# Optimization experiments

Measured on AMD Instinct MI355X. Metric: run time of the kernel, lower is better.

Reference implementation:

```python
import jax, jax.numpy as jnp
import numpy as np

ALPHA = 0.25
GAMMA = 2.0
EPS = 1e-8


def _lsa(cost):
    """Jonker-Volgenant shortest-augmenting-path linear sum assignment.
    Matches scipy.optimize.linear_sum_assignment for rectangular matrices."""
    cost = np.asarray(cost, dtype=np.float64)
    transposed = cost.shape[0] > cost.shape[1]
    if transposed:
        cost = cost.T
    n, m = cost.shape  # n <= m
    INF = 1e18
    u = np.zeros(n + 1)
    v = np.zeros(m + 1)
    p = np.zeros(m + 1, dtype=np.int64)   # p[j] = row (1-indexed) assigned to col j
    way = np.zeros(m + 1, dtype=np.int64)
    for i in range(1, n + 1):
        p[0] = i
        j0 = 0
        minv = np.full(m + 1, INF)
        used = np.zeros(m + 1, dtype=bool)
        while True:
            used[j0] = True
            i0 = p[j0]
            cur = cost[i0 - 1] - u[i0] - v[1:]
            free = ~used[1:]
            better = free & (cur < minv[1:])
            minv[1:][better] = cur[better]
            way[1:][better] = j0
            masked = np.where(free, minv[1:], INF)
            j1 = int(np.argmin(masked)) + 1
            delta = masked[j1 - 1]
            u[p[used]] += delta
            v[used] -= delta
            minv[1:][free] -= delta
            j0 = j1
            if p[j0] == 0:
                break
        while j0 != 0:  # augment
            j1 = way[j0]
            p[j0] = p[j1]
            j0 = j1
    row_of_col = p[1:] - 1
    cols = np.nonzero(row_of_col >= 0)[0]
    rows = row_of_col[cols]
    if transposed:
        rows, cols = cols, rows
    order = np.argsort(rows)
    return rows[order], cols[order]


def _focal_cost(p):
    """pos_cost - neg_cost for sigmoid probs p, per focal-loss matcher cost."""
    neg = (1.0 - ALPHA) * p ** GAMMA * (-jnp.log(1.0 - p + EPS))
    pos = ALPHA * (1.0 - p) ** GAMMA * (-jnp.log(p + EPS))
    return pos - neg


def _match(rec, loc, targets):
    """rec: [bs, Q, Crec] logits; loc: [bs, Q, Cloc] logits; targets: [bs, nt] int.
    Returns (src_idx, tgt_idx) each [bs, nt] (query index, target index)."""
    nt = targets.shape[1]
    cost_class = jnp.take_along_axis(_focal_cost(jax.nn.sigmoid(rec)),
                                     targets[:, None, :], axis=2)      # [bs, Q, nt]
    cost_pos = _focal_cost(jax.nn.sigmoid(loc))[:, :, :nt]             # tgt_pos = arange(nt)
    C = np.asarray(2.0 * cost_class + cost_pos)                        # [bs, Q, nt]
    src, tgt = [], []
    for b in range(C.shape[0]):  # per-batch Hungarian, as in original
        r, c = _lsa(C[b])
        src.append(r)
        tgt.append(c)
    return jnp.asarray(np.stack(src)), jnp.asarray(np.stack(tgt))


def _ce(logits, labels):
    # F.cross_entropy with mean reduction
    logp = jax.nn.log_softmax(logits, axis=-1)
    return -jnp.mean(jnp.take_along_axis(logp, labels[..., None], axis=-1))


def setup_inputs() -> dict:
    key = jax.random.key(0)
    k1, k2, k3 = jax.random.split(key, 3)
    rec = jax.random.normal(k1, (128, 107, 32, 32), dtype=jnp.float32)
    loc = jax.random.normal(k2, (128, 25, 32, 32), dtype=jnp.float32)
    targets = jax.random.randint(k3, (128, 25), 0, 107, dtype=jnp.int64)
    return {"rec": rec, "loc": loc, "targets": targets}


def reference(rec, loc, targets):
    bs, c_rec, H, W = rec.shape
    c_loc = loc.shape[1]
    nt = targets.shape[1]
    rec = jnp.transpose(rec.reshape(bs, c_rec, H * W), (0, 2, 1))  # [bs, Q, Crec]
    loc = jnp.transpose(loc.reshape(bs, c_loc, H * W), (0, 2, 1))  # [bs, Q, Cloc]
    src_idx, tgt_idx = _match(rec, loc, targets)                   # [bs, nt] each
    rec_m = jnp.take_along_axis(rec, src_idx[:, :, None], axis=1)  # [bs, nt, Crec]
    loc_m = jnp.take_along_axis(loc, src_idx[:, :, None], axis=1)  # [bs, nt, Cloc]
    cls_labels = jnp.take_along_axis(targets, tgt_idx, axis=1)     # [bs, nt]
    pos_labels = tgt_idx                                           # tgt_pos[b, j] == j
    det_rec_losses = _ce(rec_m.reshape(bs * nt, c_rec), cls_labels.reshape(-1))
    pos_losses = _ce(loc_m.reshape(bs * nt, c_loc), pos_labels.reshape(-1))
    return (det_rec_losses, pos_losses)
```

## Files before the change

kernel.cpp:

```cpp
#include <hip/hip_runtime.h>
#include <hip/hip_bf16.h>
#include <math.h>

#define BS   128
#define NT   25
#define CREC 107
#define CLOC 25
#define QN   1024
#define INFD 1e18
#define WSTR 257
__device__ __forceinline__ int widx(int j) {
    int q = j - 1;
    return (q & 3) * WSTR + (q >> 2);
}

__device__ __forceinline__ float focal_cost_f(float x) {
    float p   = 1.0f / (1.0f + __expf(-x));
    float neg = 0.75f * p * p * (-__logf(1.0f - p + 1e-8f));
    float pos = 0.25f * (1.0f - p) * (1.0f - p) * (-__logf(p + 1e-8f));
    return pos - neg;
}

__global__ __launch_bounds__(256)
void rowmin_kernel(const float* __restrict__ rec, const float* __restrict__ loc,
                   const int* __restrict__ targets, float* __restrict__ cost_g,
                   float* __restrict__ rowmin_g, int* __restrict__ rowarg_g) {
    const int pid   = blockIdx.x;
    const int b     = pid / NT, r = pid % NT;
    const int tid   = threadIdx.x;
    const int qbase = tid << 2;
    const int tc    = targets[pid];

    float4 r4 = *(const float4*)(rec + ((size_t)b * CREC + tc) * QN + qbase);
    float4 l4 = *(const float4*)(loc + ((size_t)b * CLOC + r)  * QN + qbase);
    float4 c;
    c.x = 2.0f * focal_cost_f(r4.x) + focal_cost_f(l4.x);
    c.y = 2.0f * focal_cost_f(r4.y) + focal_cost_f(l4.y);
    c.z = 2.0f * focal_cost_f(r4.z) + focal_cost_f(l4.z);
    c.w = 2.0f * focal_cost_f(r4.w) + focal_cost_f(l4.w);
    *(float4*)(cost_g + ((size_t)pid << 10) + qbase) = c;

    float bv = c.x; int bq = qbase;
    if (c.y < bv) { bv = c.y; bq = qbase + 1; }
    if (c.z < bv) { bv = c.z; bq = qbase + 2; }
    if (c.w < bv) { bv = c.w; bq = qbase + 3; }
    #pragma unroll
    for (int off = 32; off; off >>= 1) {
        float ov = __shfl_xor(bv, off);
        int   oq = __shfl_xor(bq, off);
        if (ov < bv || (ov == bv && oq < bq)) { bv = ov; bq = oq; }
    }
    __shared__ float bmv[4];
    __shared__ int   bmq[4];
    if ((tid & 63) == 0) { bmv[tid >> 6] = bv; bmq[tid >> 6] = bq; }
    __syncthreads();
    if (tid == 0) {
        float fv = bmv[0]; int fq = bmq[0];
        #pragma unroll
        for (int w = 1; w < 4; ++w) {
            float ov = bmv[w]; int oq = bmq[w];
            if (ov < fv || (ov == fv && oq < fq)) { fv = ov; fq = oq; }
        }
        rowmin_g[pid] = fv; rowarg_g[pid] = fq;
    }
}

__global__ __launch_bounds__(256)
void search_kernel(const float* __restrict__ cost_g,
                   const float* __restrict__ rowmin_g, const int* __restrict__ rowarg_g,
                   int* __restrict__ pairq_g) {
    const int b     = blockIdx.x;
    const int tid   = threadIdx.x;
    const int wave  = tid >> 6;
    const int lane  = tid & 63;
    const int qbase = tid << 2;

    __shared__ int    way_s[4 * WSTR];
    __shared__ int    p_s[QN + 1];
    __shared__ double u_s[NT + 1];
    __shared__ float  rowmin_s[NT];
    __shared__ int    rowarg_s[NT];
    __shared__ int    unassigned_s[NT];
    __shared__ int    nun_s;
    __shared__ double candv_s[2][4];
    __shared__ int    candj_s[2][4];

    for (int j = tid; j <= QN; j += 256) p_s[j] = 0;
    if (tid < NT) {
        rowmin_s[tid] = rowmin_g[b * NT + tid];
        rowarg_s[tid] = rowarg_g[b * NT + tid];
    }
    __syncthreads();

    if (tid == 0) {
        nun_s = 0;
        for (int r = 0; r < NT; ++r) {
            u_s[r + 1] = (double)rowmin_s[r];
            int j = rowarg_s[r] + 1;
            if (p_s[j] == 0) p_s[j] = r + 1;
            else             unassigned_s[nun_s++] = r + 1;
        }
    }
    __syncthreads();
    const int nun = nun_s;

    const float* cb = cost_g + ((size_t)b * NT << 10);

    double v[4] = {0.0, 0.0, 0.0, 0.0};

    for (int s = 0; s < nun; ++s) {
        const int i = unassigned_s[s];
        double minv[4] = {INFD, INFD, INFD, INFD};
        double snap[4] = {0.0, 0.0, 0.0, 0.0};
        double dsum    = 0.0;
        unsigned usedmask = 0;
        int j0 = 0;
        int parity = 0;

        for (;;) {
            int i0;
            if (j0 == 0) {
                i0 = i;
            } else {
                int q0 = j0 - 1;
                if ((q0 >> 2) == tid) {
                    int m = q0 & 3;
                    usedmask |= 1u << m;
                    minv[m] = INFD;
                    snap[m] = dsum;
                }
                i0 = p_s[j0];
            }
            const double ui0 = u_s[i0];
            const float4 c4 = *(const float4*)(cb + ((size_t)(i0 - 1) << 10) + qbase);
            const float cf[4] = { c4.x, c4.y, c4.z, c4.w };

            double bestv = INFD; int bestj = QN + 2;
            #pragma unroll
            for (int m = 0; m < 4; ++m) {
                if (!(usedmask & (1u << m))) {
                    const int j = qbase + m + 1;
                    double cur = (double)cf[m] - ui0 - v[m];
                    if (cur < minv[m]) { minv[m] = cur; way_s[widx(j)] = j0; }
                    double mv = minv[m];
                    if (mv < bestv || (mv == bestv && j < bestj)) { bestv = mv; bestj = j; }
                }
            }

            float own32 = (float)bestv;
            float w32 = own32;
            #pragma unroll
            for (int off = 32; off; off >>= 1) w32 = fminf(w32, __shfl_xor(w32, off));
            unsigned long long cand = __ballot(own32 == w32);
            double wv = INFD; int wj = QN + 2;
            while (cand) {
                int l = __ffsll(cand) - 1; cand &= cand - 1;
                double vv = __shfl(bestv, l);
                int    jj = __shfl(bestj, l);
                if (vv < wv || (vv == wv && jj < wj)) { wv = vv; wj = jj; }
            }
            if (lane == 0) { candv_s[parity][wave] = wv; candj_s[parity][wave] = wj; }
            __syncthreads();
            double delta = candv_s[parity][0]; int j1 = candj_s[parity][0];
            #pragma unroll
            for (int w = 1; w < 4; ++w) {
                double dv = candv_s[parity][w]; int dj = candj_s[parity][w];
                if (dv < delta || (dv == delta && dj < j1)) { delta = dv; j1 = dj; }
            }
            parity ^= 1;
            dsum += delta;

            #pragma unroll
            for (int m = 0; m < 4; ++m) {
                if (usedmask & (1u << m)) v[m]    -= delta;
                else                      minv[m] -= delta;
            }
            j0 = j1;
            if (p_s[j0] == 0) break;
        }

        if (tid == 0) u_s[i] += dsum;
        unsigned mm = usedmask;
        while (mm) {
            int m = __ffs(mm) - 1; mm &= mm - 1;
            u_s[p_s[qbase + m + 1]] += dsum - snap[m];
        }
        __syncthreads();
        if (tid == 0) {
            int jj = j0;
            while (jj != 0) {
                int jn = way_s[widx(jj)];
                p_s[jj] = (jn == 0) ? i : p_s[jn];
                jj = jn;
            }
        }
        __syncthreads();
    }

    for (int j = tid + 1; j <= QN; j += 256)
        if (p_s[j] > 0) pairq_g[b * NT + (p_s[j] - 1)] = j - 1;
}

__global__ __launch_bounds__(64)
void loss_kernel(const float* __restrict__ rec, const float* __restrict__ loc,
                 const int* __restrict__ targets, const int* __restrict__ pairq_g,
                 float* __restrict__ partial) {
    const int pid  = blockIdx.x;
    const int b    = pid / NT, t = pid % NT;
    const int lane = threadIdx.x;
    const int q    = pairq_g[pid];

    const float* rb = rec + (size_t)b * CREC * QN + q;
    float x0 = (lane < CREC)      ? rb[(size_t)lane * QN]        : -1e30f;
    float x1 = (lane + 64 < CREC) ? rb[(size_t)(lane + 64) * QN] : -1e30f;
    float mx = fmaxf(x0, x1);
    #pragma unroll
    for (int off = 32; off; off >>= 1) mx = fmaxf(mx, __shfl_xor(mx, off));
    float e = 0.0f;
    if (lane < CREC)      e += expf(x0 - mx);
    if (lane + 64 < CREC) e += expf(x1 - mx);
    #pragma unroll
    for (int off = 32; off; off >>= 1) e += __shfl_xor(e, off);
    float lse = mx + logf(e);

    const float* lb = loc + (size_t)b * CLOC * QN + q;
    float y = (lane < CLOC) ? lb[(size_t)lane * QN] : -1e30f;
    float my = y;
    #pragma unroll
    for (int off = 32; off; off >>= 1) my = fmaxf(my, __shfl_xor(my, off));
    float ey = (lane < CLOC) ? expf(y - my) : 0.0f;
    #pragma unroll
    for (int off = 32; off; off >>= 1) ey += __shfl_xor(ey, off);
    float lsey = my + logf(ey);

    if (lane == 0) {
        int lab = targets[pid];
        partial[pid]           = lse  - rb[(size_t)lab * QN];
        partial[BS * NT + pid] = lsey - lb[(size_t)t * QN];
    }
}

__global__ __launch_bounds__(256)
void finalize_kernel(const float* __restrict__ partial, float* __restrict__ out) {
    const int tid = threadIdx.x;
    float s0 = 0.0f, s1 = 0.0f;
    for (int i = tid; i < BS * NT; i += 256) {
        s0 += partial[i];
        s1 += partial[BS * NT + i];
    }
    __shared__ float a0[4], a1[4];
    #pragma unroll
    for (int off = 32; off; off >>= 1) { s0 += __shfl_xor(s0, off); s1 += __shfl_xor(s1, off); }
    if ((tid & 63) == 0) { a0[tid >> 6] = s0; a1[tid >> 6] = s1; }
    __syncthreads();
    if (tid == 0) {
        out[0] = (a0[0] + a0[1] + a0[2] + a0[3]) * (1.0f / (BS * NT));
        out[1] = (a1[0] + a1[1] + a1[2] + a1[3]) * (1.0f / (BS * NT));
    }
}

extern "C" void kernel_launch(void* const* d_in, const int* in_sizes, int n_in,
                              void* d_out, int out_size, void* d_ws, size_t ws_size,
                              hipStream_t stream) {
    (void)in_sizes; (void)n_in; (void)out_size; (void)ws_size;
    const float* rec     = (const float*)d_in[0];
    const float* loc     = (const float*)d_in[1];
    const int*   targets = (const int*)d_in[2];
    float* out = (float*)d_out;

    float* cost_g   = (float*)d_ws;
    float* rowmin_g = cost_g + (size_t)BS * NT * QN;
    int*   rowarg_g = (int*)(rowmin_g + BS * NT);
    int*   pairq_g  = rowarg_g + BS * NT;
    float* partial  = (float*)(pairq_g + BS * NT);

    hipLaunchKernelGGL(rowmin_kernel, dim3(BS * NT), dim3(256), 0, stream,
                       rec, loc, targets, cost_g, rowmin_g, rowarg_g);
    hipLaunchKernelGGL(search_kernel, dim3(BS), dim3(256), 0, stream,
                       cost_g, rowmin_g, rowarg_g, pairq_g);
    hipLaunchKernelGGL(loss_kernel, dim3(BS * NT), dim3(64), 0, stream,
                       rec, loc, targets, pairq_g, partial);
    hipLaunchKernelGGL(finalize_kernel, dim3(1), dim3(256), 0, stream,
                       partial, out);
}
```

Baseline: 142.1 us.

## Run Hungarian search with a single wavefront per batch to drop block barriers

The augmenting-path search kernel now uses one 64-lane wavefront per batch instead of four. Each lane owns 16 columns in a strided layout, so the per-step argmin reduction stays inside the wave. This removes the __syncthreads and shared-memory candidate exchange on every Dijkstra step. In exchange each lane does four times more serial column work per step and holds far more registers (16-entry double arrays). It also adds an early skip when no rows are unassigned.

```diff
diff --git a/kernel.cpp b/kernel.cpp
--- a/kernel.cpp
+++ b/kernel.cpp
@@ -8,11 +8,6 @@
 #define CLOC 25
 #define QN   1024
 #define INFD 1e18
-#define WSTR 257
-__device__ __forceinline__ int widx(int j) {
-    int q = j - 1;
-    return (q & 3) * WSTR + (q >> 2);
-}
 
 __device__ __forceinline__ float focal_cost_f(float x) {
     float p   = 1.0f / (1.0f + __expf(-x));
@@ -65,139 +60,133 @@
     }
 }
 
-__global__ __launch_bounds__(256)
+__global__ __launch_bounds__(64)
 void search_kernel(const float* __restrict__ cost_g,
                    const float* __restrict__ rowmin_g, const int* __restrict__ rowarg_g,
                    int* __restrict__ pairq_g) {
-    const int b     = blockIdx.x;
-    const int tid   = threadIdx.x;
-    const int wave  = tid >> 6;
-    const int lane  = tid & 63;
-    const int qbase = tid << 2;
-
-    __shared__ int    way_s[4 * WSTR];
+    const int b    = blockIdx.x;
+    const int lane = threadIdx.x;
+
+    __shared__ int    way_s[QN + 1];
     __shared__ int    p_s[QN + 1];
     __shared__ double u_s[NT + 1];
     __shared__ float  rowmin_s[NT];
     __shared__ int    rowarg_s[NT];
     __shared__ int    unassigned_s[NT];
     __shared__ int    nun_s;
-    __shared__ double candv_s[2][4];
-    __shared__ int    candj_s[2][4];
-
-    for (int j = tid; j <= QN; j += 256) p_s[j] = 0;
-    if (tid < NT) {
-        rowmin_s[tid] = rowmin_g[b * NT + tid];
-        rowarg_s[tid] = rowarg_g[b * NT + tid];
-    }
-    __syncthreads();
-
-    if (tid == 0) {
-        nun_s = 0;
+
+    for (int j = lane; j <= QN; j += 64) p_s[j] = 0;
+    if (lane < NT) {
+        rowmin_s[lane] = rowmin_g[b * NT + lane];
+        rowarg_s[lane] = rowarg_g[b * NT + lane];
+    }
+    __syncthreads();
+
+    if (lane == 0) {
+        int nun = 0;
         for (int r = 0; r < NT; ++r) {
             u_s[r + 1] = (double)rowmin_s[r];
             int j = rowarg_s[r] + 1;
             if (p_s[j] == 0) p_s[j] = r + 1;
-            else             unassigned_s[nun_s++] = r + 1;
+            else             unassigned_s[nun++] = r + 1;
         }
+        nun_s = nun;
     }
     __syncthreads();
     const int nun = nun_s;
 
-    const float* cb = cost_g + ((size_t)b * NT << 10);
-
-    double v[4] = {0.0, 0.0, 0.0, 0.0};
-
-    for (int s = 0; s < nun; ++s) {
-        const int i = unassigned_s[s];
-        double minv[4] = {INFD, INFD, INFD, INFD};
-        double snap[4] = {0.0, 0.0, 0.0, 0.0};
-        double dsum    = 0.0;
-        unsigned usedmask = 0;
-        int j0 = 0;
-        int parity = 0;
-
-        for (;;) {
-            int i0;
-            if (j0 == 0) {
-                i0 = i;
-            } else {
-                int q0 = j0 - 1;
-                if ((q0 >> 2) == tid) {
-                    int m = q0 & 3;
-                    usedmask |= 1u << m;
-                    minv[m] = INFD;
-                    snap[m] = dsum;
-                }
-                i0 = p_s[j0];
+    if (nun > 0) {
+        const float* cb = cost_g + ((size_t)b * NT << 10);
+        double v[16];
+        #pragma unroll
+        for (int m = 0; m < 16; ++m) v[m] = 0.0;
+
+        for (int s = 0; s < nun; ++s) {
+            const int i = unassigned_s[s];
+            double minv[16], snap[16];
+            #pragma unroll
+            for (int m = 0; m < 16; ++m) { minv[m] = INFD; snap[m] = 0.0; }
+            double dsum = 0.0;
+            unsigned usedmask = 0;
+            int j0 = 0;
+
+            for (;;) {
+                int i0;
+                if (j0 == 0) {
+                    i0 = i;
+                } else {
+                    int q0 = j0 - 1;
+                    if ((q0 & 63) == lane) {
+                        int mm = q0 >> 6;
+                        usedmask |= 1u << mm;
+                        #pragma unroll
+                        for (int m = 0; m < 16; ++m)
+                            if (m == mm) { minv[m] = INFD; snap[m] = dsum; }
+                    }
+                    i0 = p_s[j0];
+                }
+                const double ui0 = u_s[i0];
+                const float* rowp = cb + ((size_t)(i0 - 1) << 10);
+                float cf[16];
+                #pragma unroll
+                for (int m = 0; m < 16; ++m) cf[m] = rowp[(m << 6) + lane];
+
+                double bestv = INFD; int bestj = QN + 2;
+                #pragma unroll
+                for (int m = 0; m < 16; ++m) {
+                    if (!(usedmask & (1u << m))) {
+                        const int j = (m << 6) + lane + 1;
+                        double cur = (double)cf[m] - ui0 - v[m];
+                        if (cur < minv[m]) { minv[m] = cur; way_s[j] = j0; }
+                        double mv = minv[m];
+                        if (mv < bestv || (mv == bestv && j < bestj)) { bestv = mv; bestj = j; }
+                    }
+                }
+
+                float own32 = (float)bestv;
+                float w32 = own32;
+                #pragma unroll
+                for (int off = 32; off; off >>= 1) w32 = fminf(w32, __shfl_xor(w32, off));
+                unsigned long long cand = __ballot(own32 == w32);
+                double wv = INFD; int wj = QN + 2;
+                while (cand) {
+                    int l = __ffsll(cand) - 1; cand &= cand - 1;
+                    double vv = __shfl(bestv, l);
+                    int    jj = __shfl(bestj, l);
+                    if (vv < wv || (vv == wv && jj < wj)) { wv = vv; wj = jj; }
+                }
+                const double delta = wv; const int j1 = wj;
+                dsum += delta;
+
+                #pragma unroll
+                for (int m = 0; m < 16; ++m) {
+                    if (usedmask & (1u << m)) v[m]    -= delta;
+                    else                      minv[m] -= delta;
+                }
+                j0 = j1;
+                if (p_s[j0] == 0) break;
             }
-            const double ui0 = u_s[i0];
-            const float4 c4 = *(const float4*)(cb + ((size_t)(i0 - 1) << 10) + qbase);
-            const float cf[4] = { c4.x, c4.y, c4.z, c4.w };
-
-            double bestv = INFD; int bestj = QN + 2;
-            #pragma unroll
-            for (int m = 0; m < 4; ++m) {
-                if (!(usedmask & (1u << m))) {
-                    const int j = qbase + m + 1;
-                    double cur = (double)cf[m] - ui0 - v[m];
-                    if (cur < minv[m]) { minv[m] = cur; way_s[widx(j)] = j0; }
-                    double mv = minv[m];
-                    if (mv < bestv || (mv == bestv && j < bestj)) { bestv = mv; bestj = j; }
-                }
+
+            if (lane == 0) u_s[i] += dsum;
+            unsigned mm = usedmask;
+            while (mm) {
+                int m = __ffs(mm) - 1; mm &= mm - 1;
+                u_s[p_s[(m << 6) + lane + 1]] += dsum - snap[m];
             }
-
-            float own32 = (float)bestv;
-            float w32 = own32;
-            #pragma unroll
-            for (int off = 32; off; off >>= 1) w32 = fminf(w32, __shfl_xor(w32, off));
-            unsigned long long cand = __ballot(own32 == w32);
-            double wv = INFD; int wj = QN + 2;
-            while (cand) {
-                int l = __ffsll(cand) - 1; cand &= cand - 1;
-                double vv = __shfl(bestv, l);
-                int    jj = __shfl(bestj, l);
-                if (vv < wv || (vv == wv && jj < wj)) { wv = vv; wj = jj; }
+            __syncthreads();
+            if (lane == 0) {
+                int jj = j0;
+                while (jj != 0) {
+                    int jn = way_s[jj];
+                    p_s[jj] = (jn == 0) ? i : p_s[jn];
+                    jj = jn;
+                }
             }
-            if (lane == 0) { candv_s[parity][wave] = wv; candj_s[parity][wave] = wj; }
             __syncthreads();
-            double delta = candv_s[parity][0]; int j1 = candj_s[parity][0];
-            #pragma unroll
-            for (int w = 1; w < 4; ++w) {
-                double dv = candv_s[parity][w]; int dj = candj_s[parity][w];
-                if (dv < delta || (dv == delta && dj < j1)) { delta = dv; j1 = dj; }
-            }
-            parity ^= 1;
-            dsum += delta;
-
-            #pragma unroll
-            for (int m = 0; m < 4; ++m) {
-                if (usedmask & (1u << m)) v[m]    -= delta;
-                else                      minv[m] -= delta;
-            }
-            j0 = j1;
-            if (p_s[j0] == 0) break;
         }
-
-        if (tid == 0) u_s[i] += dsum;
-        unsigned mm = usedmask;
-        while (mm) {
-            int m = __ffs(mm) - 1; mm &= mm - 1;
-            u_s[p_s[qbase + m + 1]] += dsum - snap[m];
-        }
-        __syncthreads();
-        if (tid == 0) {
-            int jj = j0;
-            while (jj != 0) {
-                int jn = way_s[widx(jj)];
-                p_s[jj] = (jn == 0) ? i : p_s[jn];
-                jj = jn;
-            }
-        }
-        __syncthreads();
-    }
-
-    for (int j = tid + 1; j <= QN; j += 256)
+    }
+
+    for (int j = lane + 1; j <= QN; j += 64)
         if (p_s[j] > 0) pairq_g[b * NT + (p_s[j] - 1)] = j - 1;
 }
 
@@ -276,7 +265,7 @@
 
     hipLaunchKernelGGL(rowmin_kernel, dim3(BS * NT), dim3(256), 0, stream,
                        rec, loc, targets, cost_g, rowmin_g, rowarg_g);
-    hipLaunchKernelGGL(search_kernel, dim3(BS), dim3(256), 0, stream,
+    hipLaunchKernelGGL(search_kernel, dim3(BS), dim3(64), 0, stream,
                        cost_g, rowmin_g, rowarg_g, pairq_g);
     hipLaunchKernelGGL(loss_kernel, dim3(BS * NT), dim3(64), 0, stream,
                        rec, loc, targets, pairq_g, partial);
```

New measurement: 143.0 us. About the same (+0.6%).
